# Kernel optimization log

Hardware: AMD Instinct MI355X
Metric: run time of the kernel (lower is better)

The kernel has to match this reference:

```python
import jax, jax.numpy as jnp
import numpy as np

N, B, H, NH = 16384, 64, 256, 8
MAXN = 512
EPS = 1e-5


def setup_inputs() -> dict:
    key = jax.random.key(0)
    ks = jax.random.split(key, 8)
    s = 0.02
    return {
        "x": jax.random.normal(ks[0], (N, H), jnp.float32),
        "batch": jnp.sort(jax.random.randint(ks[1], (N,), 0, B)),
        "max_nodes": MAXN,
        "norm1_w": jnp.ones((H,), jnp.float32),
        "norm1_b": jnp.zeros((H,), jnp.float32),
        "in_proj_w": jax.random.normal(ks[2], (3 * H, H), jnp.float32) * s,
        "in_proj_b": jnp.zeros((3 * H,), jnp.float32),
        "out_proj_w": jax.random.normal(ks[3], (H, H), jnp.float32) * s,
        "out_proj_b": jnp.zeros((H,), jnp.float32),
        "norm2_w": jnp.ones((H,), jnp.float32),
        "norm2_b": jnp.zeros((H,), jnp.float32),
        "ffn_w1": jax.random.normal(ks[4], (4 * H, H), jnp.float32) * s,
        "ffn_b1": jnp.zeros((4 * H,), jnp.float32),
        "ffn_w2": jax.random.normal(ks[5], (H, 4 * H), jnp.float32) * s,
        "ffn_b2": jnp.zeros((H,), jnp.float32),
    }


def _graph_norm(x, batch, countsf, w, b):
    # Per-graph mean and unbiased std (torch.std default), eps added to std.
    mean = jax.ops.segment_sum(x, batch, num_segments=B) / countsf[:, None]
    c = x - mean[batch]
    var = jax.ops.segment_sum(c * c, batch, num_segments=B) / jnp.maximum(countsf - 1.0, 1.0)[:, None]
    std = jnp.sqrt(var) + EPS
    return w * (c / std[batch]) + b


def _forward(x, batch, max_nodes, norm1_w, norm1_b, in_proj_w, in_proj_b,
             out_proj_w, out_proj_b, norm2_w, norm2_b, ffn_w1, ffn_b1, ffn_w2, ffn_b2):
    n = x.shape[0]
    counts = jax.ops.segment_sum(jnp.ones((n,), jnp.int32), batch, num_segments=B)  # [B]
    countsf = counts.astype(x.dtype)
    starts = jnp.concatenate([jnp.zeros((1,), jnp.int32), jnp.cumsum(counts)[:-1]])
    pos = jnp.arange(n, dtype=jnp.int32) - starts[batch]  # position within graph (batch is sorted)

    # GraphNorm 1, then pack ragged -> padded [B, M, H]
    xn = _graph_norm(x, batch, countsf, norm1_w, norm1_b)
    x_pad = jnp.zeros((B, max_nodes, H), x.dtype).at[batch, pos].set(xn)
    key_valid = jnp.arange(max_nodes)[None, :] < counts[:, None]  # [B, M] True=real node

    # Multi-head attention (eval mode, key_padding_mask)
    qkv = x_pad @ in_proj_w.T + in_proj_b  # [B, M, 3H]
    q, k, v = jnp.split(qkv, 3, axis=-1)
    hd = H // NH
    heads = lambda t: t.reshape(B, max_nodes, NH, hd).transpose(0, 2, 1, 3)  # [B, NH, M, hd]
    q, k, v = heads(q), heads(k), heads(v)
    scores = jnp.einsum('bhqd,bhkd->bhqk', q, k) / np.float32(np.sqrt(hd))
    scores = jnp.where(key_valid[:, None, None, :], scores, jnp.float32(-1e9))
    attn = jax.nn.softmax(scores, axis=-1)
    ctx = jnp.einsum('bhqk,bhkd->bhqd', attn, v).transpose(0, 2, 1, 3).reshape(B, max_nodes, H)
    attn_out = ctx @ out_proj_w.T + out_proj_b

    # Unpack padded -> ragged, residual
    x = x + attn_out[batch, pos]

    # GraphNorm 2 + FFN (exact GELU) + residual
    xn2 = _graph_norm(x, batch, countsf, norm2_w, norm2_b)
    h = jax.nn.gelu(xn2 @ ffn_w1.T + ffn_b1, approximate=False)
    return x + (h @ ffn_w2.T + ffn_b2)


def reference(x, batch, max_nodes, norm1_w, norm1_b, in_proj_w, in_proj_b,
              out_proj_w, out_proj_b, norm2_w, norm2_b, ffn_w1, ffn_b1, ffn_w2, ffn_b2):
    return _forward(x, batch, max_nodes, norm1_w, norm1_b, in_proj_w, in_proj_b,
                    out_proj_w, out_proj_b, norm2_w, norm2_b, ffn_w1, ffn_b1, ffn_w2, ffn_b2)
```

## Files before the change

kernel.cpp:

```cpp
#include <hip/hip_runtime.h>
#include <hip/hip_bf16.h>
#include <math.h>

typedef __bf16 bf16;
typedef bf16 bf16x4 __attribute__((ext_vector_type(4)));
typedef bf16 bf16x8 __attribute__((ext_vector_type(8)));
typedef float f32x4 __attribute__((ext_vector_type(4)));

#define NNODES 16384
#define NB 64
#define HDIM 256
#define NHEADS 8
#define HD 32
#define GN_STRIPS 16

typedef __attribute__((address_space(3))) unsigned int lds_u32;
typedef __attribute__((address_space(1))) const unsigned int glb_u32;

__device__ __forceinline__ void async_copy16(const bf16* gsrc, bf16* ldst) {
    __builtin_amdgcn_global_load_lds((glb_u32*)gsrc, (lds_u32*)ldst, 16, 0, 0);
}

__global__ void cvt_all(const float* __restrict__ pw_q, const float* __restrict__ pw_o,
                        const float* __restrict__ pw_1, const float* __restrict__ pw_2,
                        bf16* __restrict__ dq, bf16* __restrict__ d_o,
                        bf16* __restrict__ d1, bf16* __restrict__ d2,
                        const int* __restrict__ batch, int* __restrict__ starts,
                        int* __restrict__ counts) {
    if (blockIdx.x == 0 && threadIdx.x < 64) {
        int b = threadIdx.x;
        int lo = 0, hi = NNODES;
        while (lo < hi) { int mid = (lo + hi) >> 1; if (batch[mid] < b) lo = mid + 1; else hi = mid; }
        int s0 = lo;
        lo = 0; hi = NNODES;
        while (lo < hi) { int mid = (lo + hi) >> 1; if (batch[mid] < b + 1) lo = mid + 1; else hi = mid; }
        starts[b] = s0;
        counts[b] = lo - s0;
    }
    int i = blockIdx.x * 256 + threadIdx.x;
    const float* src; bf16* dst; int j;
    if (i < 49152)       { src = pw_q; dst = dq;  j = i; }
    else if (i < 65536)  { src = pw_o; dst = d_o; j = i - 49152; }
    else if (i < 131072) { src = pw_1; dst = d1;  j = i - 65536; }
    else                 { src = pw_2; dst = d2;  j = i - 131072; }
    float4 v = *(const float4*)(src + (size_t)j * 4);
    bf16x4 o;
    o[0] = (bf16)v.x; o[1] = (bf16)v.y; o[2] = (bf16)v.z; o[3] = (bf16)v.w;
    *(bf16x4*)(dst + (size_t)j * 4) = o;
}

__global__ __launch_bounds__(256) void gn_partial(
    const float* __restrict__ x, const int* __restrict__ starts,
    const int* __restrict__ counts, float* __restrict__ part) {
    int g = blockIdx.x, strip = blockIdx.y, hh = threadIdx.x;
    int s = starts[g], c = counts[g];
    int chunk = (c + GN_STRIPS - 1) / GN_STRIPS;
    int r0 = strip * chunk, r1 = min(c, r0 + chunk);
    float sum = 0.f, sq = 0.f;
    for (int r = r0; r < r1; ++r) {
        float v = x[(size_t)(s + r) * HDIM + hh];
        sum += v; sq += v * v;
    }
    part[((size_t)(g * GN_STRIPS + strip) * 2 + 0) * HDIM + hh] = sum;
    part[((size_t)(g * GN_STRIPS + strip) * 2 + 1) * HDIM + hh] = sq;
}

__global__ __launch_bounds__(256) void gn_final(
    const float* __restrict__ part, const int* __restrict__ counts,
    const float* __restrict__ w, const float* __restrict__ b, float* __restrict__ stats) {
    int g = blockIdx.x, hh = threadIdx.x;
    float sum = 0.f, sq = 0.f;
    for (int st = 0; st < GN_STRIPS; ++st) {
        sum += part[((size_t)(g * GN_STRIPS + st) * 2 + 0) * HDIM + hh];
        sq  += part[((size_t)(g * GN_STRIPS + st) * 2 + 1) * HDIM + hh];
    }
    float cf = (float)counts[g];
    float mean = sum / cf;
    float var = (sq - cf * mean * mean) / fmaxf(cf - 1.f, 1.f);
    var = fmaxf(var, 0.f);
    float inv = 1.f / (sqrtf(var) + 1e-5f);
    float a = w[hh] * inv;
    stats[(size_t)g * 512 + hh] = a;
    stats[(size_t)g * 512 + 256 + hh] = b[hh] - mean * a;
}

__global__ __launch_bounds__(256) void gn_apply(
    const float* __restrict__ x, const int* __restrict__ batch,
    const float* __restrict__ stats, bf16* __restrict__ out) {
    size_t i = ((size_t)blockIdx.x * 256 + threadIdx.x) * 4;
    int row = (int)(i >> 8);
    int g = batch[row];
    int hh = (int)(i & 255);
    float4 xv = *(const float4*)(x + i);
    float4 av = *(const float4*)(stats + (size_t)g * 512 + hh);
    float4 bv = *(const float4*)(stats + (size_t)g * 512 + 256 + hh);
    bf16x4 o;
    o[0] = (bf16)(av.x * xv.x + bv.x);
    o[1] = (bf16)(av.y * xv.y + bv.y);
    o[2] = (bf16)(av.z * xv.z + bv.z);
    o[3] = (bf16)(av.w * xv.w + bv.w);
    *(bf16x4*)(out + i) = o;
}

template <int MODE>
__global__ __launch_bounds__(256) void gemm_tn(
    const bf16* __restrict__ A, const bf16* __restrict__ B,
    const float* __restrict__ bias, const float* __restrict__ res,
    void* __restrict__ Cout, int M, int N, int K) {
    __shared__ __align__(16) bf16 As[128 * 32];
    __shared__ __align__(16) bf16 Bs[128 * 32];
    const int row0 = blockIdx.x * 128;
    const int col0 = blockIdx.y * 128;
    const int tid = threadIdx.x;
    const int lane = tid & 63;
    const int wave = tid >> 6;
    const int wm = (wave >> 1) * 64;
    const int wn = (wave & 1) * 64;
    const int lr = lane & 15;
    const int lk = lane >> 4;
    const int c0 = tid;
    const int c1 = tid + 256;
    const int r0c = c0 >> 2, o0 = (c0 & 3) * 8;
    const int r1c = c1 >> 2, o1 = (c1 & 3) * 8;

    const bf16* Ab = A + (size_t)row0 * K;
    const bf16* Bb = B + (size_t)col0 * K;

    f32x4 acc[4][4] = {};

    for (int k0 = 0; k0 < K; k0 += 32) {
        __syncthreads();
        async_copy16(Ab + (size_t)r0c * K + k0 + o0, &As[c0 * 8]);
        async_copy16(Ab + (size_t)r1c * K + k0 + o1, &As[c1 * 8]);
        async_copy16(Bb + (size_t)r0c * K + k0 + o0, &Bs[c0 * 8]);
        async_copy16(Bb + (size_t)r1c * K + k0 + o1, &Bs[c1 * 8]);
        __syncthreads();
        bf16x8 af[4], bfr[4];
#pragma unroll
        for (int mi = 0; mi < 4; ++mi)
            af[mi] = *(const bf16x8*)&As[(wm + mi * 16 + lr) * 32 + lk * 8];
#pragma unroll
        for (int ni = 0; ni < 4; ++ni)
            bfr[ni] = *(const bf16x8*)&Bs[(wn + ni * 16 + lr) * 32 + lk * 8];
#pragma unroll
        for (int mi = 0; mi < 4; ++mi)
#pragma unroll
            for (int ni = 0; ni < 4; ++ni)
                acc[mi][ni] = __builtin_amdgcn_mfma_f32_16x16x32_bf16(af[mi], bfr[ni], acc[mi][ni], 0, 0, 0);
    }

#pragma unroll
    for (int mi = 0; mi < 4; ++mi) {
#pragma unroll
        for (int ni = 0; ni < 4; ++ni) {
            const int col = col0 + wn + ni * 16 + lr;
            const float bv = bias[col];
#pragma unroll
            for (int r = 0; r < 4; ++r) {
                const int row = row0 + wm + mi * 16 + lk * 4 + r;
                float v = acc[mi][ni][r] + bv;
                size_t idx = (size_t)row * N + col;
                if (MODE == 0) {
                    ((bf16*)Cout)[idx] = (bf16)v;
                } else if (MODE == 1) {
                    ((float*)Cout)[idx] = v + res[idx];
                } else {
                    float gel = 0.5f * v * (1.f + erff(v * 0.70710678118654752f));
                    ((bf16*)Cout)[idx] = (bf16)gel;
                }
            }
        }
    }
}

__global__ __launch_bounds__(256) void gemm_small_res(
    const bf16* __restrict__ A, const bf16* __restrict__ B,
    const float* __restrict__ bias, const float* __restrict__ res,
    float* __restrict__ Cout, int M, int N, int K) {
    __shared__ __align__(16) bf16 As[64 * 32];
    __shared__ __align__(16) bf16 Bs[64 * 32];
    const int row0 = blockIdx.x * 64;
    const int col0 = blockIdx.y * 64;
    const int tid = threadIdx.x;
    const int lane = tid & 63;
    const int wave = tid >> 6;
    const int wr = (wave >> 1) * 32;
    const int wc = (wave & 1) * 32;
    const int lr = lane & 15;
    const int lk = lane >> 4;
    const int rs = tid >> 2, os = (tid & 3) * 8;

    const bf16* Ab = A + (size_t)row0 * K;
    const bf16* Bb = B + (size_t)col0 * K;

    f32x4 acc[2][2] = {};

    for (int k0 = 0; k0 < K; k0 += 32) {
        __syncthreads();
        async_copy16(Ab + (size_t)rs * K + k0 + os, &As[tid * 8]);
        async_copy16(Bb + (size_t)rs * K + k0 + os, &Bs[tid * 8]);
        __syncthreads();
        bf16x8 af[2], bfr[2];
#pragma unroll
        for (int mi = 0; mi < 2; ++mi)
            af[mi] = *(const bf16x8*)&As[(wr + mi * 16 + lr) * 32 + lk * 8];
#pragma unroll
        for (int ni = 0; ni < 2; ++ni)
            bfr[ni] = *(const bf16x8*)&Bs[(wc + ni * 16 + lr) * 32 + lk * 8];
#pragma unroll
        for (int mi = 0; mi < 2; ++mi)
#pragma unroll
            for (int ni = 0; ni < 2; ++ni)
                acc[mi][ni] = __builtin_amdgcn_mfma_f32_16x16x32_bf16(af[mi], bfr[ni], acc[mi][ni], 0, 0, 0);
    }

#pragma unroll
    for (int mi = 0; mi < 2; ++mi) {
#pragma unroll
        for (int ni = 0; ni < 2; ++ni) {
            const int col = col0 + wc + ni * 16 + lr;
            const float bv = bias[col];
#pragma unroll
            for (int r = 0; r < 4; ++r) {
                const int row = row0 + wr + mi * 16 + lk * 4 + r;
                size_t idx = (size_t)row * N + col;
                Cout[idx] = acc[mi][ni][r] + bv + res[idx];
            }
        }
    }
}

__global__ __launch_bounds__(256) void attn_mfma(
    const bf16* __restrict__ qkv, const int* __restrict__ starts,
    const int* __restrict__ counts, bf16* __restrict__ ctx) {
    int g = blockIdx.x, h = blockIdx.y;
    int s = starts[g], c = counts[g];
    if (c <= 0) return;
    __shared__ __align__(16) bf16 Qs[256][40];
    __shared__ __align__(16) bf16 Ks[64][40];
    __shared__ __align__(16) bf16 Vt[32][72];
    __shared__ __align__(16) bf16 Ps[4][64][72];
    __shared__ float Ls[4][64];
    const int tid = threadIdx.x;
    const int w = tid >> 6, lane = tid & 63;
    const int lo = lane & 15, hi = lane >> 4;
    const float scale = 0.17677669529663687f;
    const int nqc = (c + 255) >> 8;
    const int nkt = (c + 63) >> 6;

    for (int qc = 0; qc < nqc; ++qc) {
        {
            int qrow = qc * 256 + tid;
            const bf16* qp = qkv + (size_t)(s + qrow) * 768 + h * HD;
#pragma unroll
            for (int t4 = 0; t4 < 4; ++t4) {
                bf16x8 sv;
                if (qrow < c) {
                    bf16x8 v = *(const bf16x8*)(qp + t4 * 8);
#pragma unroll
                    for (int u = 0; u < 8; ++u) sv[u] = (bf16)((float)v[u] * scale);
                } else {
#pragma unroll
                    for (int u = 0; u < 8; ++u) sv[u] = (bf16)0.f;
                }
                *(bf16x8*)&Qs[tid][t4 * 8] = sv;
            }
        }
        __syncthreads();
        bf16x8 bq[4];
#pragma unroll
        for (int nt = 0; nt < 4; ++nt) bq[nt] = *(const bf16x8*)&Qs[w * 64 + nt * 16 + lo][hi * 8];

        f32x4 ctxa[4][2] = {};
        float l[4] = {0.f, 0.f, 0.f, 0.f};

        for (int kt = 0; kt < nkt; ++kt) {
            {
                int krow = kt * 64 + (tid >> 2);
                bf16x8 v;
                if (krow < c) v = *(const bf16x8*)(qkv + (size_t)(s + krow) * 768 + 256 + h * HD + (tid & 3) * 8);
                else {
#pragma unroll
                    for (int u = 0; u < 8; ++u) v[u] = (bf16)0.f;
                }
                *(bf16x8*)&Ks[tid >> 2][(tid & 3) * 8] = v;
            }
            {
                int vrow = kt * 64 + (tid & 63);
                int dg = tid >> 6;
                bf16x8 v;
                if (vrow < c) v = *(const bf16x8*)(qkv + (size_t)(s + vrow) * 768 + 512 + h * HD + dg * 8);
                else {
#pragma unroll
                    for (int u = 0; u < 8; ++u) v[u] = (bf16)0.f;
                }
#pragma unroll
                for (int u = 0; u < 8; ++u) Vt[dg * 8 + u][tid & 63] = v[u];
            }
            __syncthreads();

            f32x4 sacc[4][4] = {};
#pragma unroll
            for (int kmt = 0; kmt < 4; ++kmt) {
                bf16x8 ak = *(const bf16x8*)&Ks[kmt * 16 + lo][hi * 8];
#pragma unroll
                for (int nt = 0; nt < 4; ++nt)
                    sacc[kmt][nt] = __builtin_amdgcn_mfma_f32_16x16x32_bf16(ak, bq[nt], sacc[kmt][nt], 0, 0, 0);
            }
#pragma unroll
            for (int kmt = 0; kmt < 4; ++kmt) {
                int kbase = kt * 64 + kmt * 16 + hi * 4;
#pragma unroll
                for (int nt = 0; nt < 4; ++nt) {
                    bf16x4 pv;
#pragma unroll
                    for (int r = 0; r < 4; ++r) {
                        float p = (kbase + r < c) ? __expf(sacc[kmt][nt][r]) : 0.f;
                        l[nt] += p;
                        pv[r] = (bf16)p;
                    }
                    *(bf16x4*)&Ps[w][nt * 16 + lo][kmt * 16 + hi * 4] = pv;
                }
            }
#pragma unroll
            for (int ks = 0; ks < 2; ++ks) {
                bf16x8 bv[2];
#pragma unroll
                for (int dn = 0; dn < 2; ++dn) bv[dn] = *(const bf16x8*)&Vt[dn * 16 + lo][ks * 32 + hi * 8];
#pragma unroll
                for (int qmt = 0; qmt < 4; ++qmt) {
                    bf16x8 ap = *(const bf16x8*)&Ps[w][qmt * 16 + lo][ks * 32 + hi * 8];
#pragma unroll
                    for (int dn = 0; dn < 2; ++dn)
                        ctxa[qmt][dn] = __builtin_amdgcn_mfma_f32_16x16x32_bf16(ap, bv[dn], ctxa[qmt][dn], 0, 0, 0);
                }
            }
            __syncthreads();
        }

#pragma unroll
        for (int nt = 0; nt < 4; ++nt) {
            l[nt] += __shfl_xor(l[nt], 16);
            l[nt] += __shfl_xor(l[nt], 32);
        }
        if (hi == 0) {
#pragma unroll
            for (int nt = 0; nt < 4; ++nt) Ls[w][nt * 16 + lo] = l[nt];
        }
#pragma unroll
        for (int qmt = 0; qmt < 4; ++qmt) {
#pragma unroll
            for (int r = 0; r < 4; ++r) {
                int qrow = qc * 256 + w * 64 + qmt * 16 + hi * 4 + r;
                if (qrow < c) {
                    float linv = 1.f / Ls[w][qmt * 16 + hi * 4 + r];
                    bf16* op = ctx + (size_t)(s + qrow) * HDIM + h * HD;
#pragma unroll
                    for (int dn = 0; dn < 2; ++dn)
                        op[dn * 16 + lo] = (bf16)(ctxa[qmt][dn][r] * linv);
                }
            }
        }
        __syncthreads();
    }
}

extern "C" void kernel_launch(void* const* d_in, const int* in_sizes, int n_in,
                              void* d_out, int out_size, void* d_ws, size_t ws_size,
                              hipStream_t stream) {
    const float* x        = (const float*)d_in[0];
    const int*   batch    = (const int*)d_in[1];
    const float* norm1_w  = (const float*)d_in[3];
    const float* norm1_b  = (const float*)d_in[4];
    const float* in_proj_w  = (const float*)d_in[5];
    const float* in_proj_b  = (const float*)d_in[6];
    const float* out_proj_w = (const float*)d_in[7];
    const float* out_proj_b = (const float*)d_in[8];
    const float* norm2_w  = (const float*)d_in[9];
    const float* norm2_b  = (const float*)d_in[10];
    const float* ffn_w1   = (const float*)d_in[11];
    const float* ffn_b1   = (const float*)d_in[12];
    const float* ffn_w2   = (const float*)d_in[13];
    const float* ffn_b2   = (const float*)d_in[14];
    float* out = (float*)d_out;

    char* ws = (char*)d_ws;
    size_t off = 0;
    auto alloc = [&](size_t bytes) -> void* {
        void* p = ws + off;
        off += bytes;
        off = (off + 255) & ~(size_t)255;
        return p;
    };
    int*  starts = (int*)alloc(NB * 4);
    int*  counts = (int*)alloc(NB * 4);
    bf16* wq = (bf16*)alloc((size_t)768 * 256 * 2);
    bf16* wo = (bf16*)alloc((size_t)256 * 256 * 2);
    bf16* w1 = (bf16*)alloc((size_t)1024 * 256 * 2);
    bf16* w2 = (bf16*)alloc((size_t)256 * 1024 * 2);
    bf16* t0  = (bf16*)alloc((size_t)NNODES * HDIM * 2);
    bf16* qkv = (bf16*)alloc((size_t)NNODES * 768 * 2);
    float* y  = (float*)alloc((size_t)NNODES * HDIM * 4);
    bf16* hbuf = (bf16*)alloc((size_t)NNODES * 1024 * 2);
    float* gnpart = (float*)alloc((size_t)NB * GN_STRIPS * 2 * HDIM * 4);
    float* gnstats = (float*)alloc((size_t)NB * 512 * 4);

    cvt_all<<<196608 / 256, 256, 0, stream>>>(in_proj_w, out_proj_w, ffn_w1, ffn_w2,
                                              wq, wo, w1, w2, batch, starts, counts);
    gn_partial<<<dim3(NB, GN_STRIPS), 256, 0, stream>>>(x, starts, counts, gnpart);
    gn_final<<<NB, 256, 0, stream>>>(gnpart, counts, norm1_w, norm1_b, gnstats);
    gn_apply<<<NNODES * HDIM / 1024, 256, 0, stream>>>(x, batch, gnstats, t0);
    gemm_tn<0><<<dim3(NNODES / 128, 768 / 128), 256, 0, stream>>>(
        t0, wq, in_proj_b, nullptr, qkv, NNODES, 768, 256);
    attn_mfma<<<dim3(NB, NHEADS), 256, 0, stream>>>(qkv, starts, counts, t0);
    gemm_small_res<<<dim3(NNODES / 64, 256 / 64), 256, 0, stream>>>(
        t0, wo, out_proj_b, x, y, NNODES, 256, 256);
    gn_partial<<<dim3(NB, GN_STRIPS), 256, 0, stream>>>(y, starts, counts, gnpart);
    gn_final<<<NB, 256, 0, stream>>>(gnpart, counts, norm2_w, norm2_b, gnstats);
    gn_apply<<<NNODES * HDIM / 1024, 256, 0, stream>>>(y, batch, gnstats, t0);
    gemm_tn<2><<<dim3(NNODES / 128, 1024 / 128), 256, 0, stream>>>(
        t0, w1, ffn_b1, nullptr, hbuf, NNODES, 1024, 256);
    gemm_small_res<<<dim3(NNODES / 64, 256 / 64), 256, 0, stream>>>(
        hbuf, w2, ffn_b2, y, out, NNODES, 256, 1024);
}
```

Baseline: 237.2 us.

## Split attention query chunks across grid and shrink GEMM row tiles

```diff
diff --git a/kernel.cpp b/kernel.cpp
--- a/kernel.cpp
+++ b/kernel.cpp
@@ -103,67 +103,60 @@
 }
 
 template <int MODE>
-__global__ __launch_bounds__(256) void gemm_tn(
+__global__ __launch_bounds__(256) void gemm_tn64(
     const bf16* __restrict__ A, const bf16* __restrict__ B,
-    const float* __restrict__ bias, const float* __restrict__ res,
-    void* __restrict__ Cout, int M, int N, int K) {
-    __shared__ __align__(16) bf16 As[128 * 32];
+    const float* __restrict__ bias, void* __restrict__ Cout,
+    int M, int N, int K) {
+    __shared__ __align__(16) bf16 As[64 * 32];
     __shared__ __align__(16) bf16 Bs[128 * 32];
-    const int row0 = blockIdx.x * 128;
+    const int row0 = blockIdx.x * 64;
     const int col0 = blockIdx.y * 128;
     const int tid = threadIdx.x;
     const int lane = tid & 63;
     const int wave = tid >> 6;
-    const int wm = (wave >> 1) * 64;
-    const int wn = (wave & 1) * 64;
+    const int wn = wave * 32;
     const int lr = lane & 15;
     const int lk = lane >> 4;
-    const int c0 = tid;
-    const int c1 = tid + 256;
-    const int r0c = c0 >> 2, o0 = (c0 & 3) * 8;
-    const int r1c = c1 >> 2, o1 = (c1 & 3) * 8;
+    const int ra = tid >> 2, oa = (tid & 3) * 8;
 
     const bf16* Ab = A + (size_t)row0 * K;
     const bf16* Bb = B + (size_t)col0 * K;
 
-    f32x4 acc[4][4] = {};
+    f32x4 acc[4][2] = {};
 
     for (int k0 = 0; k0 < K; k0 += 32) {
         __syncthreads();
-        async_copy16(Ab + (size_t)r0c * K + k0 + o0, &As[c0 * 8]);
-        async_copy16(Ab + (size_t)r1c * K + k0 + o1, &As[c1 * 8]);
-        async_copy16(Bb + (size_t)r0c * K + k0 + o0, &Bs[c0 * 8]);
-        async_copy16(Bb + (size_t)r1c * K + k0 + o1, &Bs[c1 * 8]);
-        __syncthreads();
-        bf16x8 af[4], bfr[4];
+        async_copy16(Ab + (size_t)ra * K + k0 + oa, &As[tid * 8]);
+        async_copy16(Bb + (size_t)ra * K + k0 + oa, &Bs[tid * 8]);
+        async_copy16(Bb + (size_t)(ra + 64) * K + k0 + oa, &Bs[(tid + 256) * 8]);
+        __syncthreads();
+        bf16x8 af[4], bfr[2];
 #pragma unroll
         for (int mi = 0; mi < 4; ++mi)
-            af[mi] = *(const bf16x8*)&As[(wm + mi * 16 + lr) * 32 + lk * 8];
-#pragma unroll
-        for (int ni = 0; ni < 4; ++ni)
+            af[mi] = *(const bf16x8*)&As[(mi * 16 + lr) * 32 + lk * 8];
+#pragma unroll
+        for (int ni = 0; ni < 2; ++ni)
             bfr[ni] = *(const bf16x8*)&Bs[(wn + ni * 16 + lr) * 32 + lk * 8];
 #pragma unroll
         for (int mi = 0; mi < 4; ++mi)
 #pragma unroll
-            for (int ni = 0; ni < 4; ++ni)
+            for (int ni = 0; ni < 2; ++ni)
                 acc[mi][ni] = __builtin_amdgcn_mfma_f32_16x16x32_bf16(af[mi], bfr[ni], acc[mi][ni], 0, 0, 0);
     }
 
 #pragma unroll
     for (int mi = 0; mi < 4; ++mi) {
 #pragma unroll
-        for (int ni = 0; ni < 4; ++ni) {
+        for (int ni = 0; ni < 2; ++ni) {
             const int col = col0 + wn + ni * 16 + lr;
             const float bv = bias[col];
 #pragma unroll
             for (int r = 0; r < 4; ++r) {
-                const int row = row0 + wm + mi * 16 + lk * 4 + r;
+                const int row = row0 + mi * 16 + lk * 4 + r;
                 float v = acc[mi][ni][r] + bv;
                 size_t idx = (size_t)row * N + col;
                 if (MODE == 0) {
                     ((bf16*)Cout)[idx] = (bf16)v;
-                } else if (MODE == 1) {
-                    ((float*)Cout)[idx] = v + res[idx];
                 } else {
                     float gel = 0.5f * v * (1.f + erff(v * 0.70710678118654752f));
                     ((bf16*)Cout)[idx] = (bf16)gel;
@@ -233,9 +226,9 @@
 __global__ __launch_bounds__(256) void attn_mfma(
     const bf16* __restrict__ qkv, const int* __restrict__ starts,
     const int* __restrict__ counts, bf16* __restrict__ ctx) {
-    int g = blockIdx.x, h = blockIdx.y;
+    int g = blockIdx.x, h = blockIdx.y, qc = blockIdx.z;
     int s = starts[g], c = counts[g];
-    if (c <= 0) return;
+    if (qc * 256 >= c) return;
     __shared__ __align__(16) bf16 Qs[256][40];
     __shared__ __align__(16) bf16 Ks[64][40];
     __shared__ __align__(16) bf16 Vt[32][72];
@@ -245,123 +238,119 @@
     const int w = tid >> 6, lane = tid & 63;
     const int lo = lane & 15, hi = lane >> 4;
     const float scale = 0.17677669529663687f;
-    const int nqc = (c + 255) >> 8;
     const int nkt = (c + 63) >> 6;
 
-    for (int qc = 0; qc < nqc; ++qc) {
+    {
+        int qrow = qc * 256 + tid;
+        const bf16* qp = qkv + (size_t)(s + qrow) * 768 + h * HD;
+#pragma unroll
+        for (int t4 = 0; t4 < 4; ++t4) {
+            bf16x8 sv;
+            if (qrow < c) {
+                bf16x8 v = *(const bf16x8*)(qp + t4 * 8);
+#pragma unroll
+                for (int u = 0; u < 8; ++u) sv[u] = (bf16)((float)v[u] * scale);
+            } else {
+#pragma unroll
+                for (int u = 0; u < 8; ++u) sv[u] = (bf16)0.f;
+            }
+            *(bf16x8*)&Qs[tid][t4 * 8] = sv;
+        }
+    }
+    __syncthreads();
+    bf16x8 bq[4];
+#pragma unroll
+    for (int nt = 0; nt < 4; ++nt) bq[nt] = *(const bf16x8*)&Qs[w * 64 + nt * 16 + lo][hi * 8];
+
+    f32x4 ctxa[4][2] = {};
+    float l[4] = {0.f, 0.f, 0.f, 0.f};
+
+    for (int kt = 0; kt < nkt; ++kt) {
         {
-            int qrow = qc * 256 + tid;
-            const bf16* qp = qkv + (size_t)(s + qrow) * 768 + h * HD;
-#pragma unroll
-            for (int t4 = 0; t4 < 4; ++t4) {
-                bf16x8 sv;
-                if (qrow < c) {
-                    bf16x8 v = *(const bf16x8*)(qp + t4 * 8);
-#pragma unroll
-                    for (int u = 0; u < 8; ++u) sv[u] = (bf16)((float)v[u] * scale);
-                } else {
-#pragma unroll
-                    for (int u = 0; u < 8; ++u) sv[u] = (bf16)0.f;
+            int krow = kt * 64 + (tid >> 2);
+            bf16x8 v;
+            if (krow < c) v = *(const bf16x8*)(qkv + (size_t)(s + krow) * 768 + 256 + h * HD + (tid & 3) * 8);
+            else {
+#pragma unroll
+                for (int u = 0; u < 8; ++u) v[u] = (bf16)0.f;
+            }
+            *(bf16x8*)&Ks[tid >> 2][(tid & 3) * 8] = v;
+        }
+        {
+            int vrow = kt * 64 + (tid & 63);
+            int dg = tid >> 6;
+            bf16x8 v;
+            if (vrow < c) v = *(const bf16x8*)(qkv + (size_t)(s + vrow) * 768 + 512 + h * HD + dg * 8);
+            else {
+#pragma unroll
+                for (int u = 0; u < 8; ++u) v[u] = (bf16)0.f;
+            }
+#pragma unroll
+            for (int u = 0; u < 8; ++u) Vt[dg * 8 + u][tid & 63] = v[u];
+        }
+        __syncthreads();
+
+        f32x4 sacc[4][4] = {};
+#pragma unroll
+        for (int kmt = 0; kmt < 4; ++kmt) {
+            bf16x8 ak = *(const bf16x8*)&Ks[kmt * 16 + lo][hi * 8];
+#pragma unroll
+            for (int nt = 0; nt < 4; ++nt)
+                sacc[kmt][nt] = __builtin_amdgcn_mfma_f32_16x16x32_bf16(ak, bq[nt], sacc[kmt][nt], 0, 0, 0);
+        }
+#pragma unroll
+        for (int kmt = 0; kmt < 4; ++kmt) {
+            int kbase = kt * 64 + kmt * 16 + hi * 4;
+#pragma unroll
+            for (int nt = 0; nt < 4; ++nt) {
+                bf16x4 pv;
+#pragma unroll
+                for (int r = 0; r < 4; ++r) {
+                    float p = (kbase + r < c) ? __expf(sacc[kmt][nt][r]) : 0.f;
+                    l[nt] += p;
+                    pv[r] = (bf16)p;
                 }
-                *(bf16x8*)&Qs[tid][t4 * 8] = sv;
-            }
-        }
-        __syncthreads();
-        bf16x8 bq[4];
-#pragma unroll
-        for (int nt = 0; nt < 4; ++nt) bq[nt] = *(const bf16x8*)&Qs[w * 64 + nt * 16 + lo][hi * 8];
-
-        f32x4 ctxa[4][2] = {};
-        float l[4] = {0.f, 0.f, 0.f, 0.f};
-
-        for (int kt = 0; kt < nkt; ++kt) {
-            {
-                int krow = kt * 64 + (tid >> 2);
-                bf16x8 v;
-                if (krow < c) v = *(const bf16x8*)(qkv + (size_t)(s + krow) * 768 + 256 + h * HD + (tid & 3) * 8);
-                else {
-#pragma unroll
-                    for (int u = 0; u < 8; ++u) v[u] = (bf16)0.f;
-                }
-                *(bf16x8*)&Ks[tid >> 2][(tid & 3) * 8] = v;
-            }
-            {
-                int vrow = kt * 64 + (tid & 63);
-                int dg = tid >> 6;
-                bf16x8 v;
-                if (vrow < c) v = *(const bf16x8*)(qkv + (size_t)(s + vrow) * 768 + 512 + h * HD + dg * 8);
-                else {
-#pragma unroll
-                    for (int u = 0; u < 8; ++u) v[u] = (bf16)0.f;
-                }
-#pragma unroll
-                for (int u = 0; u < 8; ++u) Vt[dg * 8 + u][tid & 63] = v[u];
-            }
-            __syncthreads();
-
-            f32x4 sacc[4][4] = {};
-#pragma unroll
-            for (int kmt = 0; kmt < 4; ++kmt) {
-                bf16x8 ak = *(const bf16x8*)&Ks[kmt * 16 + lo][hi * 8];
-#pragma unroll
-                for (int nt = 0; nt < 4; ++nt)
-                    sacc[kmt][nt] = __builtin_amdgcn_mfma_f32_16x16x32_bf16(ak, bq[nt], sacc[kmt][nt], 0, 0, 0);
-            }
-#pragma unroll
-            for (int kmt = 0; kmt < 4; ++kmt) {
-                int kbase = kt * 64 + kmt * 16 + hi * 4;
-#pragma unroll
-                for (int nt = 0; nt < 4; ++nt) {
-                    bf16x4 pv;
-#pragma unroll
-                    for (int r = 0; r < 4; ++r) {
-                        float p = (kbase + r < c) ? __expf(sacc[kmt][nt][r]) : 0.f;
-                        l[nt] += p;
-                        pv[r] = (bf16)p;
-                    }
-                    *(bf16x4*)&Ps[w][nt * 16 + lo][kmt * 16 + hi * 4] = pv;
-                }
-            }
-#pragma unroll
-            for (int ks = 0; ks < 2; ++ks) {
-                bf16x8 bv[2];
-#pragma unroll
-                for (int dn = 0; dn < 2; ++dn) bv[dn] = *(const bf16x8*)&Vt[dn * 16 + lo][ks * 32 + hi * 8];
-#pragma unroll
-                for (int qmt = 0; qmt < 4; ++qmt) {
-                    bf16x8 ap = *(const bf16x8*)&Ps[w][qmt * 16 + lo][ks * 32 + hi * 8];
-#pragma unroll
-                    for (int dn = 0; dn < 2; ++dn)
-                        ctxa[qmt][dn] = __builtin_amdgcn_mfma_f32_16x16x32_bf16(ap, bv[dn], ctxa[qmt][dn], 0, 0, 0);
-                }
-            }
-            __syncthreads();
-        }
-
-#pragma unroll
-        for (int nt = 0; nt < 4; ++nt) {
-            l[nt] += __shfl_xor(l[nt], 16);
-            l[nt] += __shfl_xor(l[nt], 32);
-        }
-        if (hi == 0) {
-#pragma unroll
-            for (int nt = 0; nt < 4; ++nt) Ls[w][nt * 16 + lo] = l[nt];
-        }
-#pragma unroll
-        for (int qmt = 0; qmt < 4; ++qmt) {
-#pragma unroll
-            for (int r = 0; r < 4; ++r) {
-                int qrow = qc * 256 + w * 64 + qmt * 16 + hi * 4 + r;
-                if (qrow < c) {
-                    float linv = 1.f / Ls[w][qmt * 16 + hi * 4 + r];
-                    bf16* op = ctx + (size_t)(s + qrow) * HDIM + h * HD;
-#pragma unroll
-                    for (int dn = 0; dn < 2; ++dn)
-                        op[dn * 16 + lo] = (bf16)(ctxa[qmt][dn][r] * linv);
-                }
-            }
-        }
-        __syncthreads();
+                *(bf16x4*)&Ps[w][nt * 16 + lo][kmt * 16 + hi * 4] = pv;
+            }
+        }
+#pragma unroll
+        for (int ks = 0; ks < 2; ++ks) {
+            bf16x8 bv[2];
+#pragma unroll
+            for (int dn = 0; dn < 2; ++dn) bv[dn] = *(const bf16x8*)&Vt[dn * 16 + lo][ks * 32 + hi * 8];
+#pragma unroll
+            for (int qmt = 0; qmt < 4; ++qmt) {
+                bf16x8 ap = *(const bf16x8*)&Ps[w][qmt * 16 + lo][ks * 32 + hi * 8];
+#pragma unroll
+                for (int dn = 0; dn < 2; ++dn)
+                    ctxa[qmt][dn] = __builtin_amdgcn_mfma_f32_16x16x32_bf16(ap, bv[dn], ctxa[qmt][dn], 0, 0, 0);
+            }
+        }
+        __syncthreads();
+    }
+
+#pragma unroll
+    for (int nt = 0; nt < 4; ++nt) {
+        l[nt] += __shfl_xor(l[nt], 16);
+        l[nt] += __shfl_xor(l[nt], 32);
+    }
+    if (hi == 0) {
+#pragma unroll
+        for (int nt = 0; nt < 4; ++nt) Ls[w][nt * 16 + lo] = l[nt];
+    }
+#pragma unroll
+    for (int qmt = 0; qmt < 4; ++qmt) {
+#pragma unroll
+        for (int r = 0; r < 4; ++r) {
+            int qrow = qc * 256 + w * 64 + qmt * 16 + hi * 4 + r;
+            if (qrow < c) {
+                float linv = 1.f / Ls[w][qmt * 16 + hi * 4 + r];
+                bf16* op = ctx + (size_t)(s + qrow) * HDIM + h * HD;
+#pragma unroll
+                for (int dn = 0; dn < 2; ++dn)
+                    op[dn * 16 + lo] = (bf16)(ctxa[qmt][dn][r] * linv);
+            }
+        }
     }
 }
 
@@ -410,16 +399,16 @@
     gn_partial<<<dim3(NB, GN_STRIPS), 256, 0, stream>>>(x, starts, counts, gnpart);
     gn_final<<<NB, 256, 0, stream>>>(gnpart, counts, norm1_w, norm1_b, gnstats);
     gn_apply<<<NNODES * HDIM / 1024, 256, 0, stream>>>(x, batch, gnstats, t0);
-    gemm_tn<0><<<dim3(NNODES / 128, 768 / 128), 256, 0, stream>>>(
-        t0, wq, in_proj_b, nullptr, qkv, NNODES, 768, 256);
-    attn_mfma<<<dim3(NB, NHEADS), 256, 0, stream>>>(qkv, starts, counts, t0);
+    gemm_tn64<0><<<dim3(NNODES / 64, 768 / 128), 256, 0, stream>>>(
+        t0, wq, in_proj_b, qkv, NNODES, 768, 256);
+    attn_mfma<<<dim3(NB, NHEADS, 2), 256, 0, stream>>>(qkv, starts, counts, t0);
     gemm_small_res<<<dim3(NNODES / 64, 256 / 64), 256, 0, stream>>>(
         t0, wo, out_proj_b, x, y, NNODES, 256, 256);
     gn_partial<<<dim3(NB, GN_STRIPS), 256, 0, stream>>>(y, starts, counts, gnpart);
     gn_final<<<NB, 256, 0, stream>>>(gnpart, counts, norm2_w, norm2_b, gnstats);
     gn_apply<<<NNODES * HDIM / 1024, 256, 0, stream>>>(y, batch, gnstats, t0);
-    gemm_tn<2><<<dim3(NNODES / 128, 1024 / 128), 256, 0, stream>>>(
-        t0, w1, ffn_b1, nullptr, hbuf, NNODES, 1024, 256);
+    gemm_tn64<2><<<dim3(NNODES / 64, 1024 / 128), 256, 0, stream>>>(
+        t0, w1, ffn_b1, hbuf, NNODES, 1024, 256);
     gemm_small_res<<<dim3(NNODES / 64, 256 / 64), 256, 0, stream>>>(
         hbuf, w2, ffn_b2, y, out, NNODES, 256, 1024);
 }
```

Measured after the change: 230.9 us. -2.6%, faster.
